# Kernel optimization log

Hardware: AMD Instinct MI355X
Metric: run time of the kernel (lower is better)

The kernel has to match this reference:

```python
import jax, jax.numpy as jnp
import numpy as np

EPS = jnp.float16(1e-8)

def setup_inputs() -> dict:
    key = jax.random.key(0)
    k1, k2, k3, k4 = jax.random.split(key, 4)
    B, S, D_IN, D_OUT = 4, 2048, 4096, 4096
    x = jax.random.normal(k1, (B, S, D_IN), dtype=jnp.float16)
    weight = jax.random.randint(k2, (D_OUT, D_IN), -127, 127, dtype=jnp.int32).astype(jnp.int8)
    weight_scales = (jax.random.uniform(k3, (D_OUT,), dtype=jnp.float32) * 0.02 + 0.001).astype(jnp.float16)
    bias = (jax.random.normal(k4, (1, D_OUT), dtype=jnp.float32) * 0.01).astype(jnp.float16)
    return {"x": x, "weight": weight, "weight_scales": weight_scales, "bias": bias}

def fake_quant_per_token(x):
    # per-token absmax fake quant to int8 range, stays fp16
    scales = jnp.max(jnp.abs(x), axis=-1, keepdims=True) / jnp.float16(127.0)
    scales = jnp.maximum(scales, EPS)
    return jnp.round(x / scales) * scales

def reference(x, weight, weight_scales, bias):
    # dequantize int8 weight with per-output-channel scales -> fp16 [out, in]
    w_fp16 = weight.astype(jnp.float16) * weight_scales[:, None]
    xq = fake_quant_per_token(x)
    # y = xq @ w^T + bias  : [B, S, out]
    y = jnp.einsum('bsi,oi->bso', xq, w_fp16) + bias
    return y
```

## Files before the change

kernel.cpp:

```cpp
#include <hip/hip_runtime.h>
#include <hip/hip_fp16.h>
#include <stdint.h>

#define M_TOK 8192
#define KD 4096
#define ND 4096

using i32x4 = __attribute__((ext_vector_type(4))) int;

typedef const __attribute__((address_space(1))) void* gp_t;
typedef __attribute__((address_space(3))) void* lp_t;

__global__ __launch_bounds__(256) void prep_kernel(
    const float* __restrict__ x,
    int8_t* __restrict__ q,
    float* __restrict__ scales,
    const int* __restrict__ w32,
    int8_t* __restrict__ w8)
{
    const int t = threadIdx.x;
    if (blockIdx.x >= 8192) {
        const int b = blockIdx.x - 8192;
        const int4* w4 = (const int4*)w32;
        int* q32 = (int*)w8;
        #pragma unroll
        for (int u = 0; u < 4; ++u) {
            int g = b * 1024 + u * 256 + t;
            int4 a = w4[g];
            q32[g] = (a.x & 255) | ((a.y & 255) << 8) | ((a.z & 255) << 16) | (a.w << 24);
        }
        return;
    }

    const int row  = blockIdx.x;
    const int lane = t & 63;
    const int wave = t >> 6;

    const float4* xr = (const float4*)(x + (size_t)row * KD);
    float4 p[4];
    #pragma unroll
    for (int i = 0; i < 4; ++i) p[i] = xr[i * 256 + t];

    float am = 0.0f;
    #pragma unroll
    for (int i = 0; i < 4; ++i) {
        am = fmaxf(am, fmaxf(fmaxf(fabsf(p[i].x), fabsf(p[i].y)),
                             fmaxf(fabsf(p[i].z), fabsf(p[i].w))));
    }
    #pragma unroll
    for (int off = 32; off >= 1; off >>= 1)
        am = fmaxf(am, __shfl_xor(am, off));

    __shared__ float smax[4];
    if (lane == 0) smax[wave] = am;
    __syncthreads();
    am = fmaxf(fmaxf(smax[0], smax[1]), fmaxf(smax[2], smax[3]));

    float s = __half2float(__float2half(am * (1.0f / 127.0f)));
    s = fmaxf(s, 1e-30f);
    const float inv = 1.0f / s;

    int* qr = (int*)(q + (size_t)row * KD);
    #pragma unroll
    for (int i = 0; i < 4; ++i) {
        float vv[4] = {p[i].x, p[i].y, p[i].z, p[i].w};
        int w32v = 0;
        #pragma unroll
        for (int e = 0; e < 4; ++e) {
            float tq = __half2float(__float2half(vv[e] * inv));
            int qi = (int)rintf(tq);
            qi = max(-127, min(127, qi));
            w32v |= (qi & 255) << (8 * e);
        }
        qr[i * 256 + t] = w32v;
    }
    if (t == 0) scales[row] = s;
}


template<int MH>
__device__ __forceinline__ void read_A(const char* lA, int wr, int lane, i32x4 (&a)[4][2]) {
    const int l15 = lane & 15;
    const int cg  = (lane >> 4) << 4;
    #pragma unroll
    for (int mf = 0; mf < 4; ++mf) {
        const int row = MH * 128 + wr * 64 + mf * 16 + l15;
        const int sw  = (row & 7) << 4;
        #pragma unroll
        for (int ks = 0; ks < 2; ++ks)
            a[mf][ks] = *(const i32x4*)(lA + row * 128 + ((ks * 64 + cg) ^ sw));
    }
}

template<int NH>
__device__ __forceinline__ void read_B(const char* lB, int wc, int lane, i32x4 (&b)[2][2]) {
    const int l15 = lane & 15;
    const int cg  = (lane >> 4) << 4;
    #pragma unroll
    for (int nf = 0; nf < 2; ++nf) {
        const int row = NH * 128 + wc * 32 + nf * 16 + l15;
        const int sw  = (row & 7) << 4;
        #pragma unroll
        for (int ks = 0; ks < 2; ++ks)
            b[nf][ks] = *(const i32x4*)(lB + row * 128 + ((ks * 64 + cg) ^ sw));
    }
}

template<int MH>
__device__ __forceinline__ void mfma_half(i32x4 (&acc)[2][4][2][2],
                                          const i32x4 (&a)[4][2],
                                          const i32x4 (&b0)[2][2],
                                          const i32x4 (&b1)[2][2]) {
    __builtin_amdgcn_s_setprio(1);
    #pragma unroll
    for (int ks = 0; ks < 2; ++ks)
        #pragma unroll
        for (int mf = 0; mf < 4; ++mf) {
            #pragma unroll
            for (int nf = 0; nf < 2; ++nf)
                acc[MH][mf][0][nf] =
                    __builtin_amdgcn_mfma_i32_16x16x64_i8(a[mf][ks], b0[nf][ks],
                                                          acc[MH][mf][0][nf], 0, 0, 0);
            #pragma unroll
            for (int nf = 0; nf < 2; ++nf)
                acc[MH][mf][1][nf] =
                    __builtin_amdgcn_mfma_i32_16x16x64_i8(a[mf][ks], b1[nf][ks],
                                                          acc[MH][mf][1][nf], 0, 0, 0);
        }
    __builtin_amdgcn_s_setprio(0);
}

#define BAR() do { __builtin_amdgcn_s_barrier(); __builtin_amdgcn_sched_barrier(0); } while (0)

__global__ __launch_bounds__(512, 2) void gemm_q8_4ph_kernel(
    const int8_t* __restrict__ q,
    const int8_t* __restrict__ w8,
    const float* __restrict__ qs,
    const float* __restrict__ wscale,
    const float* __restrict__ bias,
    float* __restrict__ y)
{
    __shared__ char lds[2][2][32768];

    const int tid  = threadIdx.x;
    const int lane = tid & 63;
    const int wave = tid >> 6;
    const int wr   = wave >> 2;
    const int wc   = wave & 3;
    const int tn   = blockIdx.x;
    const int tm   = blockIdx.y;

    const int8_t* gA = q  + (size_t)(tm * 256) * KD;
    const int8_t* gB = w8 + (size_t)(tn * 256) * KD;

    char* lA0 = &lds[0][0][0]; char* lB0 = &lds[0][1][0];
    char* lA1 = &lds[1][0][0]; char* lB1 = &lds[1][1][0];

    int goff[2];
    #pragma unroll
    for (int qq = 0; qq < 2; ++qq) {
        const int d = qq * 8192 + wave * 1024 + lane * 16;
        const int r = d >> 7;
        const int cs = (d & 127) ^ ((r & 7) << 4);
        goff[qq] = r * KD + cs;
    }
    const int ldso = wave * 1024;

    #define STAGE(gbase, half, kbyte, ldst)                                              \
        do {                                                                             \
            const int8_t* _s = (gbase) + (size_t)(half) * 128 * KD + (kbyte);            \
            __builtin_amdgcn_global_load_lds((gp_t)(_s + goff[0]),                       \
                (lp_t)((ldst) + (half) * 16384 + ldso), 16, 0, 0);                       \
            __builtin_amdgcn_global_load_lds((gp_t)(_s + goff[1]),                       \
                (lp_t)((ldst) + (half) * 16384 + 8192 + ldso), 16, 0, 0);                \
        } while (0)

    i32x4 acc[2][4][2][2] = {};
    i32x4 a[4][2], b0[2][2], b1[2][2];

    STAGE(gA, 0, 0,   lA0);
    STAGE(gB, 0, 0,   lB0);
    STAGE(gA, 1, 0,   lA0);
    STAGE(gB, 1, 0,   lB0);
    STAGE(gA, 0, 128, lA1);
    STAGE(gB, 0, 128, lB1);
    asm volatile("s_waitcnt vmcnt(4)");
    BAR();

    for (int it = 0; it < 16; ++it) {
        const int kt  = 2 * it;
        const int kb1 = ((kt + 1) & 31) * 128;
        const int kb2 = ((kt + 2) & 31) * 128;
        const int kb3 = ((kt + 3) & 31) * 128;

        read_A<0>(lA0, wr, lane, a);
        read_B<0>(lB0, wc, lane, b0);
        read_B<1>(lB0, wc, lane, b1);
        STAGE(gA, 1, kb1, lA1);
        STAGE(gB, 1, kb1, lB1);
        BAR();
        mfma_half<0>(acc, a, b0, b1);
        BAR();

        read_A<1>(lA0, wr, lane, a);
        STAGE(gA, 0, kb2, lA0);
        STAGE(gB, 0, kb2, lB0);
        BAR();
        mfma_half<1>(acc, a, b0, b1);
        asm volatile("s_waitcnt vmcnt(4)");
        BAR();

        read_A<0>(lA1, wr, lane, a);
        read_B<0>(lB1, wc, lane, b0);
        read_B<1>(lB1, wc, lane, b1);
        STAGE(gA, 1, kb2, lA0);
        STAGE(gB, 1, kb2, lB0);
        BAR();
        mfma_half<0>(acc, a, b0, b1);
        BAR();

        read_A<1>(lA1, wr, lane, a);
        STAGE(gA, 0, kb3, lA1);
        STAGE(gB, 0, kb3, lB1);
        BAR();
        mfma_half<1>(acc, a, b0, b1);
        asm volatile("s_waitcnt vmcnt(4)");
        BAR();
    }
    asm volatile("s_waitcnt vmcnt(0)");

    #pragma unroll
    for (int mh = 0; mh < 2; ++mh)
        #pragma unroll
        for (int mf = 0; mf < 4; ++mf) {
            const int rm = tm * 256 + mh * 128 + wr * 64 + mf * 16 + ((lane >> 4) << 2);
            float qsv[4];
            #pragma unroll
            for (int r = 0; r < 4; ++r) qsv[r] = qs[rm + r];
            #pragma unroll
            for (int nh = 0; nh < 2; ++nh)
                #pragma unroll
                for (int nf = 0; nf < 2; ++nf) {
                    const int n = tn * 256 + nh * 128 + wc * 32 + nf * 16 + (lane & 15);
                    const float wn = wscale[n];
                    const float bn = bias[n];
                    #pragma unroll
                    for (int r = 0; r < 4; ++r)
                        y[(size_t)(rm + r) * ND + n] =
                            (float)acc[mh][mf][nh][nf][r] * (qsv[r] * wn) + bn;
                }
        }
    #undef STAGE
}

__global__ __launch_bounds__(256, 2) void gemm_q8_fallback(
    const int8_t* __restrict__ q,
    const int* __restrict__ w32,
    const float* __restrict__ qs,
    const float* __restrict__ wscale,
    const float* __restrict__ bias,
    float* __restrict__ y)
{
    __shared__ int8_t lA[128 * 64];
    __shared__ int8_t lB[128 * 64];

    const int tid  = threadIdx.x;
    const int lane = tid & 63;
    const int wave = tid >> 6;
    const int wr   = wave >> 1;
    const int wc   = wave & 1;
    const int tn   = blockIdx.x;
    const int tm   = blockIdx.y;

    const int ci0  = wave * 2;
    const int off0 = ci0 * 1024 + lane * 16;
    const int r0   = off0 >> 6;
    const int c0   = off0 & 63;
    const int off1 = off0 + 1024;
    const int r1   = off1 >> 6;
    const int c1   = off1 & 63;

    const int8_t* gA0 = q + (size_t)(tm * 128 + r0) * KD + c0;
    const int8_t* gA1 = q + (size_t)(tm * 128 + r1) * KD + c1;

    const int brow  = tid >> 1;
    const int bhalf = tid & 1;
    const int* gW = w32 + (size_t)(tn * 128 + brow) * KD + bhalf * 32;

    i32x4 acc[4][4] = {};
    const int kc = (lane >> 4) * 16;
    const int rA = wr * 64 + (lane & 15);
    const int rB = wc * 64 + (lane & 15);

    for (int k0 = 0; k0 < KD; k0 += 64) {
        __builtin_amdgcn_global_load_lds((gp_t)(gA0 + k0), (lp_t)(lA + ci0 * 1024),        16, 0, 0);
        __builtin_amdgcn_global_load_lds((gp_t)(gA1 + k0), (lp_t)(lA + ci0 * 1024 + 1024), 16, 0, 0);
        int bw[8];
        #pragma unroll
        for (int u = 0; u < 8; ++u) {
            i32x4 a4 = *(const i32x4*)(gW + k0 + u * 4);
            bw[u] = (a4[0] & 255) | ((a4[1] & 255) << 8) | ((a4[2] & 255) << 16) | (a4[3] << 24);
        }
        *(i32x4*)(lB + brow * 64 + bhalf * 32)      = i32x4{bw[0], bw[1], bw[2], bw[3]};
        *(i32x4*)(lB + brow * 64 + bhalf * 32 + 16) = i32x4{bw[4], bw[5], bw[6], bw[7]};
        __syncthreads();

        i32x4 a[4], b[4];
        #pragma unroll
        for (int i = 0; i < 4; ++i) a[i] = *(const i32x4*)(lA + (rA + i * 16) * 64 + kc);
        #pragma unroll
        for (int j = 0; j < 4; ++j) b[j] = *(const i32x4*)(lB + (rB + j * 16) * 64 + kc);
        #pragma unroll
        for (int i = 0; i < 4; ++i)
            #pragma unroll
            for (int j = 0; j < 4; ++j)
                acc[i][j] = __builtin_amdgcn_mfma_i32_16x16x64_i8(a[i], b[j], acc[i][j], 0, 0, 0);
        __syncthreads();
    }

    const int cbase = tn * 128 + wc * 64 + (lane & 15);
    const int rbase = tm * 128 + wr * 64 + ((lane >> 4) << 2);
    #pragma unroll
    for (int j = 0; j < 4; ++j) {
        const int n  = cbase + j * 16;
        const float wn = wscale[n];
        const float bn = bias[n];
        #pragma unroll
        for (int i = 0; i < 4; ++i)
            #pragma unroll
            for (int r = 0; r < 4; ++r) {
                const int m = rbase + i * 16 + r;
                y[(size_t)m * ND + n] = (float)acc[i][j][r] * (qs[m] * wn) + bn;
            }
    }
}

extern "C" void kernel_launch(void* const* d_in, const int* in_sizes, int n_in,
                              void* d_out, int out_size, void* d_ws, size_t ws_size,
                              hipStream_t stream) {
    const float* x      = (const float*)d_in[0];
    const int*   w32    = (const int*)d_in[1];
    const float* wscale = (const float*)d_in[2];
    const float* bias   = (const float*)d_in[3];
    float*       y      = (float*)d_out;

    const size_t q_bytes  = (size_t)M_TOK * KD;
    const size_t s_bytes  = (size_t)M_TOK * sizeof(float);
    const size_t w8_bytes = (size_t)ND * KD;

    int8_t* qbuf   = (int8_t*)d_ws;
    float*  scales = (float*)((char*)d_ws + q_bytes);
    int8_t* w8     = (int8_t*)((char*)d_ws + q_bytes + s_bytes);

    if (ws_size >= q_bytes + s_bytes + w8_bytes) {
        prep_kernel<<<8192 + 4096, 256, 0, stream>>>(x, qbuf, scales, w32, w8);
        dim3 grid(ND / 256, M_TOK / 256);
        gemm_q8_4ph_kernel<<<grid, 512, 0, stream>>>(qbuf, w8, scales, wscale, bias, y);
    } else {
        prep_kernel<<<8192, 256, 0, stream>>>(x, qbuf, scales, w32, w8);
        dim3 grid(ND / 128, M_TOK / 128);
        gemm_q8_fallback<<<grid, 256, 0, stream>>>(qbuf, w32, scales, wscale, bias, y);
    }
}
```

Before: 181.9 us.

## Switch int8 GEMM from 16x16x64 to 32x32x32 MFMA tiles

Replaces the 16x16x64 int8 MFMA instructions with 32x32x32 int8 MFMA. Each wave now covers a 64x64 N-slice per M-half instead of two 32-wide N-halves. The LDS read patterns, the per-wave tile mapping and the epilogue indexing are rewritten to match the 32x32 accumulator layout. The aim is to cut LDS operand reads per MAC and reuse B fragments across both M-halves. The risk is that the larger accumulator vectors raise register pressure and change LDS bank access.

```diff
diff --git a/kernel.cpp b/kernel.cpp
--- a/kernel.cpp
+++ b/kernel.cpp
@@ -6,7 +6,8 @@
 #define KD 4096
 #define ND 4096
 
-using i32x4 = __attribute__((ext_vector_type(4))) int;
+using i32x4  = __attribute__((ext_vector_type(4))) int;
+using i32x16 = __attribute__((ext_vector_type(16))) int;
 
 typedef const __attribute__((address_space(1))) void* gp_t;
 typedef __attribute__((address_space(3))) void* lp_t;
@@ -79,60 +80,52 @@
 
 
 template<int MH>
-__device__ __forceinline__ void read_A(const char* lA, int wr, int lane, i32x4 (&a)[4][2]) {
-    const int l15 = lane & 15;
-    const int cg  = (lane >> 4) << 4;
-    #pragma unroll
-    for (int mf = 0; mf < 4; ++mf) {
-        const int row = MH * 128 + wr * 64 + mf * 16 + l15;
+__device__ __forceinline__ void read_A32(const char* lA, int wr, int lane, i32x4 (&a)[2][4]) {
+    const int l31 = lane & 31;
+    const int kc  = (lane >> 5) << 4;
+    #pragma unroll
+    for (int mf = 0; mf < 2; ++mf) {
+        const int row = MH * 128 + wr * 64 + mf * 32 + l31;
         const int sw  = (row & 7) << 4;
         #pragma unroll
-        for (int ks = 0; ks < 2; ++ks)
-            a[mf][ks] = *(const i32x4*)(lA + row * 128 + ((ks * 64 + cg) ^ sw));
-    }
-}
-
-template<int NH>
-__device__ __forceinline__ void read_B(const char* lB, int wc, int lane, i32x4 (&b)[2][2]) {
-    const int l15 = lane & 15;
-    const int cg  = (lane >> 4) << 4;
+        for (int ks = 0; ks < 4; ++ks)
+            a[mf][ks] = *(const i32x4*)(lA + row * 128 + ((ks * 32 + kc) ^ sw));
+    }
+}
+
+__device__ __forceinline__ void read_B32(const char* lB, int wc, int lane, i32x4 (&b)[2][4]) {
+    const int l31 = lane & 31;
+    const int kc  = (lane >> 5) << 4;
     #pragma unroll
     for (int nf = 0; nf < 2; ++nf) {
-        const int row = NH * 128 + wc * 32 + nf * 16 + l15;
+        const int row = wc * 64 + nf * 32 + l31;
         const int sw  = (row & 7) << 4;
         #pragma unroll
-        for (int ks = 0; ks < 2; ++ks)
-            b[nf][ks] = *(const i32x4*)(lB + row * 128 + ((ks * 64 + cg) ^ sw));
+        for (int ks = 0; ks < 4; ++ks)
+            b[nf][ks] = *(const i32x4*)(lB + row * 128 + ((ks * 32 + kc) ^ sw));
     }
 }
 
 template<int MH>
-__device__ __forceinline__ void mfma_half(i32x4 (&acc)[2][4][2][2],
-                                          const i32x4 (&a)[4][2],
-                                          const i32x4 (&b0)[2][2],
-                                          const i32x4 (&b1)[2][2]) {
+__device__ __forceinline__ void mfma_half32(i32x16 (&acc)[2][2][2],
+                                            const i32x4 (&a)[2][4],
+                                            const i32x4 (&b)[2][4]) {
     __builtin_amdgcn_s_setprio(1);
     #pragma unroll
-    for (int ks = 0; ks < 2; ++ks)
-        #pragma unroll
-        for (int mf = 0; mf < 4; ++mf) {
+    for (int ks = 0; ks < 4; ++ks)
+        #pragma unroll
+        for (int mf = 0; mf < 2; ++mf)
             #pragma unroll
             for (int nf = 0; nf < 2; ++nf)
-                acc[MH][mf][0][nf] =
-                    __builtin_amdgcn_mfma_i32_16x16x64_i8(a[mf][ks], b0[nf][ks],
-                                                          acc[MH][mf][0][nf], 0, 0, 0);
-            #pragma unroll
-            for (int nf = 0; nf < 2; ++nf)
-                acc[MH][mf][1][nf] =
-                    __builtin_amdgcn_mfma_i32_16x16x64_i8(a[mf][ks], b1[nf][ks],
-                                                          acc[MH][mf][1][nf], 0, 0, 0);
-        }
+                acc[MH][mf][nf] =
+                    __builtin_amdgcn_mfma_i32_32x32x32_i8(a[mf][ks], b[nf][ks],
+                                                          acc[MH][mf][nf], 0, 0, 0);
     __builtin_amdgcn_s_setprio(0);
 }
 
 #define BAR() do { __builtin_amdgcn_s_barrier(); __builtin_amdgcn_sched_barrier(0); } while (0)
 
-__global__ __launch_bounds__(512, 2) void gemm_q8_4ph_kernel(
+__global__ __launch_bounds__(512, 2) void gemm_q8_32x32_kernel(
     const int8_t* __restrict__ q,
     const int8_t* __restrict__ w8,
     const float* __restrict__ qs,
@@ -175,8 +168,8 @@
                 (lp_t)((ldst) + (half) * 16384 + 8192 + ldso), 16, 0, 0);                \
         } while (0)
 
-    i32x4 acc[2][4][2][2] = {};
-    i32x4 a[4][2], b0[2][2], b1[2][2];
+    i32x16 acc[2][2][2] = {};
+    i32x4 a[2][4], b[2][4];
 
     STAGE(gA, 0, 0,   lA0);
     STAGE(gB, 0, 0,   lB0);
@@ -193,37 +186,35 @@
         const int kb2 = ((kt + 2) & 31) * 128;
         const int kb3 = ((kt + 3) & 31) * 128;
 
-        read_A<0>(lA0, wr, lane, a);
-        read_B<0>(lB0, wc, lane, b0);
-        read_B<1>(lB0, wc, lane, b1);
+        read_A32<0>(lA0, wr, lane, a);
+        read_B32(lB0, wc, lane, b);
         STAGE(gA, 1, kb1, lA1);
         STAGE(gB, 1, kb1, lB1);
         BAR();
-        mfma_half<0>(acc, a, b0, b1);
-        BAR();
-
-        read_A<1>(lA0, wr, lane, a);
+        mfma_half32<0>(acc, a, b);
+        BAR();
+
+        read_A32<1>(lA0, wr, lane, a);
         STAGE(gA, 0, kb2, lA0);
         STAGE(gB, 0, kb2, lB0);
         BAR();
-        mfma_half<1>(acc, a, b0, b1);
+        mfma_half32<1>(acc, a, b);
         asm volatile("s_waitcnt vmcnt(4)");
         BAR();
 
-        read_A<0>(lA1, wr, lane, a);
-        read_B<0>(lB1, wc, lane, b0);
-        read_B<1>(lB1, wc, lane, b1);
+        read_A32<0>(lA1, wr, lane, a);
+        read_B32(lB1, wc, lane, b);
         STAGE(gA, 1, kb2, lA0);
         STAGE(gB, 1, kb2, lB0);
         BAR();
-        mfma_half<0>(acc, a, b0, b1);
-        BAR();
-
-        read_A<1>(lA1, wr, lane, a);
+        mfma_half32<0>(acc, a, b);
+        BAR();
+
+        read_A32<1>(lA1, wr, lane, a);
         STAGE(gA, 0, kb3, lA1);
         STAGE(gB, 0, kb3, lB1);
         BAR();
-        mfma_half<1>(acc, a, b0, b1);
+        mfma_half32<1>(acc, a, b);
         asm volatile("s_waitcnt vmcnt(4)");
         BAR();
     }
@@ -232,23 +223,24 @@
     #pragma unroll
     for (int mh = 0; mh < 2; ++mh)
         #pragma unroll
-        for (int mf = 0; mf < 4; ++mf) {
-            const int rm = tm * 256 + mh * 128 + wr * 64 + mf * 16 + ((lane >> 4) << 2);
-            float qsv[4];
-            #pragma unroll
-            for (int r = 0; r < 4; ++r) qsv[r] = qs[rm + r];
-            #pragma unroll
-            for (int nh = 0; nh < 2; ++nh)
+        for (int mf = 0; mf < 2; ++mf) {
+            const int rbase = tm * 256 + mh * 128 + wr * 64 + mf * 32 + ((lane >> 5) << 2);
+            float qsv[16];
+            #pragma unroll
+            for (int reg = 0; reg < 16; ++reg)
+                qsv[reg] = qs[rbase + (reg & 3) + 8 * (reg >> 2)];
+            #pragma unroll
+            for (int nf = 0; nf < 2; ++nf) {
+                const int n = tn * 256 + wc * 64 + nf * 32 + (lane & 31);
+                const float wn = wscale[n];
+                const float bn = bias[n];
                 #pragma unroll
-                for (int nf = 0; nf < 2; ++nf) {
-                    const int n = tn * 256 + nh * 128 + wc * 32 + nf * 16 + (lane & 15);
-                    const float wn = wscale[n];
-                    const float bn = bias[n];
-                    #pragma unroll
-                    for (int r = 0; r < 4; ++r)
-                        y[(size_t)(rm + r) * ND + n] =
-                            (float)acc[mh][mf][nh][nf][r] * (qsv[r] * wn) + bn;
+                for (int reg = 0; reg < 16; ++reg) {
+                    const int m = rbase + (reg & 3) + 8 * (reg >> 2);
+                    y[(size_t)m * ND + n] =
+                        (float)acc[mh][mf][nf][reg] * (qsv[reg] * wn) + bn;
                 }
+            }
         }
     #undef STAGE
 }
@@ -355,7 +347,7 @@
     if (ws_size >= q_bytes + s_bytes + w8_bytes) {
         prep_kernel<<<8192 + 4096, 256, 0, stream>>>(x, qbuf, scales, w32, w8);
         dim3 grid(ND / 256, M_TOK / 256);
-        gemm_q8_4ph_kernel<<<grid, 512, 0, stream>>>(qbuf, w8, scales, wscale, bias, y);
+        gemm_q8_32x32_kernel<<<grid, 512, 0, stream>>>(qbuf, w8, scales, wscale, bias, y);
     } else {
         prep_kernel<<<8192, 256, 0, stream>>>(x, qbuf, scales, w32, w8);
         dim3 grid(ND / 128, M_TOK / 128);
```

New measurement: 196.9 us. 8.2% more time.

## Peel final K iteration and stage epilogue through swizzled LDS for vector stores

Applied to the files above, without the earlier changes.

The last main-loop iteration is peeled so it no longer issues wrap-around prefetches of K tiles that are never used. The epilogue writes scaled accumulators into a per-wave XOR-swizzled LDS region. It then reads them back as 16-byte rows and writes coalesced float4 nontemporal stores to the output, instead of scattered 4-byte stores. This cuts wasted global loads and improves write coalescing, at the cost of extra LDS traffic and barriers in the epilogue.

```diff
diff --git a/kernel.cpp b/kernel.cpp
--- a/kernel.cpp
+++ b/kernel.cpp
@@ -7,6 +7,7 @@
 #define ND 4096
 
 using i32x4 = __attribute__((ext_vector_type(4))) int;
+using f32x4 = __attribute__((ext_vector_type(4))) float;
 
 typedef const __attribute__((address_space(1))) void* gp_t;
 typedef __attribute__((address_space(3))) void* lp_t;
@@ -187,11 +188,11 @@
     asm volatile("s_waitcnt vmcnt(4)");
     BAR();
 
-    for (int it = 0; it < 16; ++it) {
+    for (int it = 0; it < 15; ++it) {
         const int kt  = 2 * it;
-        const int kb1 = ((kt + 1) & 31) * 128;
-        const int kb2 = ((kt + 2) & 31) * 128;
-        const int kb3 = ((kt + 3) & 31) * 128;
+        const int kb1 = (kt + 1) * 128;
+        const int kb2 = (kt + 2) * 128;
+        const int kb3 = (kt + 3) * 128;
 
         read_A<0>(lA0, wr, lane, a);
         read_B<0>(lB0, wc, lane, b0);
@@ -227,29 +228,77 @@
         asm volatile("s_waitcnt vmcnt(4)");
         BAR();
     }
-    asm volatile("s_waitcnt vmcnt(0)");
-
-    #pragma unroll
-    for (int mh = 0; mh < 2; ++mh)
-        #pragma unroll
-        for (int mf = 0; mf < 4; ++mf) {
-            const int rm = tm * 256 + mh * 128 + wr * 64 + mf * 16 + ((lane >> 4) << 2);
-            float qsv[4];
-            #pragma unroll
-            for (int r = 0; r < 4; ++r) qsv[r] = qs[rm + r];
-            #pragma unroll
-            for (int nh = 0; nh < 2; ++nh)
+
+    {
+        const int kb1 = 31 * 128;
+        read_A<0>(lA0, wr, lane, a);
+        read_B<0>(lB0, wc, lane, b0);
+        read_B<1>(lB0, wc, lane, b1);
+        STAGE(gA, 1, kb1, lA1);
+        STAGE(gB, 1, kb1, lB1);
+        BAR();
+        mfma_half<0>(acc, a, b0, b1);
+        BAR();
+
+        read_A<1>(lA0, wr, lane, a);
+        BAR();
+        mfma_half<1>(acc, a, b0, b1);
+        asm volatile("s_waitcnt vmcnt(0)");
+        BAR();
+
+        read_A<0>(lA1, wr, lane, a);
+        read_B<0>(lB1, wc, lane, b0);
+        read_B<1>(lB1, wc, lane, b1);
+        BAR();
+        mfma_half<0>(acc, a, b0, b1);
+        BAR();
+
+        read_A<1>(lA1, wr, lane, a);
+        BAR();
+        mfma_half<1>(acc, a, b0, b1);
+        BAR();
+    }
+
+    {
+        char* myl = &lds[0][0][0] + wave * 16384;
+        const int g   = lane >> 4;
+        const int l15 = lane & 15;
+        #pragma unroll
+        for (int nh = 0; nh < 2; ++nh) {
+            #pragma unroll
+            for (int mh = 0; mh < 2; ++mh)
                 #pragma unroll
-                for (int nf = 0; nf < 2; ++nf) {
-                    const int n = tn * 256 + nh * 128 + wc * 32 + nf * 16 + (lane & 15);
-                    const float wn = wscale[n];
-                    const float bn = bias[n];
+                for (int mf = 0; mf < 4; ++mf) {
+                    const int rmb = tm * 256 + mh * 128 + wr * 64 + mf * 16 + g * 4;
+                    float qsv[4];
                     #pragma unroll
-                    for (int r = 0; r < 4; ++r)
-                        y[(size_t)(rm + r) * ND + n] =
-                            (float)acc[mh][mf][nh][nf][r] * (qsv[r] * wn) + bn;
+                    for (int r = 0; r < 4; ++r) qsv[r] = qs[rmb + r];
+                    #pragma unroll
+                    for (int nf = 0; nf < 2; ++nf) {
+                        const int n  = tn * 256 + nh * 128 + wc * 32 + nf * 16 + l15;
+                        const float wn = wscale[n];
+                        const float bn = bias[n];
+                        const int cl = nf * 16 + l15;
+                        #pragma unroll
+                        for (int r = 0; r < 4; ++r) {
+                            const int rl = mh * 64 + mf * 16 + g * 4 + r;
+                            const float val = (float)acc[mh][mf][nh][nf][r] * (qsv[r] * wn) + bn;
+                            *(float*)(myl + rl * 128 + ((cl * 4) ^ ((rl & 7) << 4))) = val;
+                        }
+                    }
                 }
+            __builtin_amdgcn_s_barrier();
+            const int gcol = tn * 256 + nh * 128 + wc * 32 + (lane & 7) * 4;
+            #pragma unroll
+            for (int k = 0; k < 16; ++k) {
+                const int rl = (lane >> 3) + k * 8;
+                const f32x4 v = *(const f32x4*)(myl + rl * 128 + (((lane & 7) * 16) ^ ((rl & 7) << 4)));
+                const int grow = tm * 256 + (rl >> 6) * 128 + wr * 64 + (rl & 63);
+                __builtin_nontemporal_store(v, (f32x4*)(y + (size_t)grow * ND + gcol));
+            }
+            __builtin_amdgcn_s_barrier();
         }
+    }
     #undef STAGE
 }
 
```

Result: faster. 167.8 us (-7.8%).

## Replace 256x256 8-wave GEMM with 128x128 4-wave tile and LDS-staged epilogue

Applied to the files above, without the earlier changes.

Swaps the 256x256-tile, 512-thread int8 GEMM for a 128x128-tile, 256-thread kernel. Each wave now computes a 64x64 sub-tile over a simpler two-phase double-buffered loop with explicit lgkm/vm waits. The epilogue is rewritten to stage the scaled outputs through swizzled LDS and write them with coalesced 16-byte nontemporal stores. The smaller tile roughly doubles global operand traffic per FLOP and reduces reuse, in exchange for more blocks, smaller LDS use and better store coalescing.

```diff
diff --git a/kernel.cpp b/kernel.cpp
--- a/kernel.cpp
+++ b/kernel.cpp
@@ -7,6 +7,7 @@
 #define ND 4096
 
 using i32x4 = __attribute__((ext_vector_type(4))) int;
+using f32x4 = __attribute__((ext_vector_type(4))) float;
 
 typedef const __attribute__((address_space(1))) void* gp_t;
 typedef __attribute__((address_space(3))) void* lp_t;
@@ -78,13 +79,12 @@
 }
 
 
-template<int MH>
-__device__ __forceinline__ void read_A(const char* lA, int wr, int lane, i32x4 (&a)[4][2]) {
+__device__ __forceinline__ void read_Af(const char* lA, int wr, int lane, i32x4 (&a)[4][2]) {
     const int l15 = lane & 15;
     const int cg  = (lane >> 4) << 4;
     #pragma unroll
     for (int mf = 0; mf < 4; ++mf) {
-        const int row = MH * 128 + wr * 64 + mf * 16 + l15;
+        const int row = wr * 64 + mf * 16 + l15;
         const int sw  = (row & 7) << 4;
         #pragma unroll
         for (int ks = 0; ks < 2; ++ks)
@@ -92,13 +92,12 @@
     }
 }
 
-template<int NH>
-__device__ __forceinline__ void read_B(const char* lB, int wc, int lane, i32x4 (&b)[2][2]) {
+__device__ __forceinline__ void read_Bf(const char* lB, int wc, int lane, i32x4 (&b)[4][2]) {
     const int l15 = lane & 15;
     const int cg  = (lane >> 4) << 4;
     #pragma unroll
-    for (int nf = 0; nf < 2; ++nf) {
-        const int row = NH * 128 + wc * 32 + nf * 16 + l15;
+    for (int nf = 0; nf < 4; ++nf) {
+        const int row = wc * 64 + nf * 16 + l15;
         const int sw  = (row & 7) << 4;
         #pragma unroll
         for (int ks = 0; ks < 2; ++ks)
@@ -106,33 +105,26 @@
     }
 }
 
-template<int MH>
-__device__ __forceinline__ void mfma_half(i32x4 (&acc)[2][4][2][2],
-                                          const i32x4 (&a)[4][2],
-                                          const i32x4 (&b0)[2][2],
-                                          const i32x4 (&b1)[2][2]) {
+__device__ __forceinline__ void mfma_32(i32x4 (&acc)[4][4],
+                                        const i32x4 (&a)[4][2],
+                                        const i32x4 (&b)[4][2]) {
     __builtin_amdgcn_s_setprio(1);
     #pragma unroll
     for (int ks = 0; ks < 2; ++ks)
         #pragma unroll
-        for (int mf = 0; mf < 4; ++mf) {
-            #pragma unroll
-            for (int nf = 0; nf < 2; ++nf)
-                acc[MH][mf][0][nf] =
-                    __builtin_amdgcn_mfma_i32_16x16x64_i8(a[mf][ks], b0[nf][ks],
-                                                          acc[MH][mf][0][nf], 0, 0, 0);
-            #pragma unroll
-            for (int nf = 0; nf < 2; ++nf)
-                acc[MH][mf][1][nf] =
-                    __builtin_amdgcn_mfma_i32_16x16x64_i8(a[mf][ks], b1[nf][ks],
-                                                          acc[MH][mf][1][nf], 0, 0, 0);
-        }
+        for (int mf = 0; mf < 4; ++mf)
+            #pragma unroll
+            for (int nf = 0; nf < 4; ++nf)
+                acc[mf][nf] = __builtin_amdgcn_mfma_i32_16x16x64_i8(a[mf][ks], b[nf][ks],
+                                                                    acc[mf][nf], 0, 0, 0);
     __builtin_amdgcn_s_setprio(0);
 }
 
-#define BAR() do { __builtin_amdgcn_s_barrier(); __builtin_amdgcn_sched_barrier(0); } while (0)
-
-__global__ __launch_bounds__(512, 2) void gemm_q8_4ph_kernel(
+#define BAR()   __builtin_amdgcn_s_barrier()
+#define LGKM0() asm volatile("s_waitcnt lgkmcnt(0)" ::: "memory")
+#define VM8()   asm volatile("s_waitcnt vmcnt(8)")
+
+__global__ __launch_bounds__(256, 2) void gemm_q8_128_kernel(
     const int8_t* __restrict__ q,
     const int8_t* __restrict__ w8,
     const float* __restrict__ qs,
@@ -140,116 +132,113 @@
     const float* __restrict__ bias,
     float* __restrict__ y)
 {
-    __shared__ char lds[2][2][32768];
+    __shared__ char lds[2][2][16384];
 
     const int tid  = threadIdx.x;
     const int lane = tid & 63;
     const int wave = tid >> 6;
-    const int wr   = wave >> 2;
-    const int wc   = wave & 3;
+    const int wr   = wave >> 1;
+    const int wc   = wave & 1;
     const int tn   = blockIdx.x;
     const int tm   = blockIdx.y;
 
-    const int8_t* gA = q  + (size_t)(tm * 256) * KD;
-    const int8_t* gB = w8 + (size_t)(tn * 256) * KD;
+    const int8_t* gA = q  + (size_t)(tm * 128) * KD;
+    const int8_t* gB = w8 + (size_t)(tn * 128) * KD;
 
     char* lA0 = &lds[0][0][0]; char* lB0 = &lds[0][1][0];
     char* lA1 = &lds[1][0][0]; char* lB1 = &lds[1][1][0];
 
-    int goff[2];
-    #pragma unroll
-    for (int qq = 0; qq < 2; ++qq) {
-        const int d = qq * 8192 + wave * 1024 + lane * 16;
+    int goff[4];
+    #pragma unroll
+    for (int ch = 0; ch < 4; ++ch) {
+        const int d = ch * 4096 + tid * 16;
         const int r = d >> 7;
         const int cs = (d & 127) ^ ((r & 7) << 4);
-        goff[qq] = r * KD + cs;
-    }
-    const int ldso = wave * 1024;
-
-    #define STAGE(gbase, half, kbyte, ldst)                                              \
+        goff[ch] = r * KD + cs;
+    }
+    const int ldso = tid * 16;
+
+    #define STAGE(gbase, kbyte, ldst)                                                    \
         do {                                                                             \
-            const int8_t* _s = (gbase) + (size_t)(half) * 128 * KD + (kbyte);            \
-            __builtin_amdgcn_global_load_lds((gp_t)(_s + goff[0]),                       \
-                (lp_t)((ldst) + (half) * 16384 + ldso), 16, 0, 0);                       \
-            __builtin_amdgcn_global_load_lds((gp_t)(_s + goff[1]),                       \
-                (lp_t)((ldst) + (half) * 16384 + 8192 + ldso), 16, 0, 0);                \
+            const int8_t* _s = (gbase) + (kbyte);                                        \
+            __builtin_amdgcn_global_load_lds((gp_t)(_s + goff[0]), (lp_t)((ldst) + ldso),            16, 0, 0); \
+            __builtin_amdgcn_global_load_lds((gp_t)(_s + goff[1]), (lp_t)((ldst) + 4096 + ldso),     16, 0, 0); \
+            __builtin_amdgcn_global_load_lds((gp_t)(_s + goff[2]), (lp_t)((ldst) + 8192 + ldso),     16, 0, 0); \
+            __builtin_amdgcn_global_load_lds((gp_t)(_s + goff[3]), (lp_t)((ldst) + 12288 + ldso),    16, 0, 0); \
         } while (0)
 
-    i32x4 acc[2][4][2][2] = {};
-    i32x4 a[4][2], b0[2][2], b1[2][2];
-
-    STAGE(gA, 0, 0,   lA0);
-    STAGE(gB, 0, 0,   lB0);
-    STAGE(gA, 1, 0,   lA0);
-    STAGE(gB, 1, 0,   lB0);
-    STAGE(gA, 0, 128, lA1);
-    STAGE(gB, 0, 128, lB1);
-    asm volatile("s_waitcnt vmcnt(4)");
+    i32x4 acc[4][4] = {};
+    i32x4 a[4][2], b[4][2];
+
+    STAGE(gA, 0,   lA0);
+    STAGE(gB, 0,   lB0);
+    STAGE(gA, 128, lA1);
+    STAGE(gB, 128, lB1);
+    VM8();
     BAR();
 
     for (int it = 0; it < 16; ++it) {
         const int kt  = 2 * it;
-        const int kb1 = ((kt + 1) & 31) * 128;
         const int kb2 = ((kt + 2) & 31) * 128;
         const int kb3 = ((kt + 3) & 31) * 128;
 
-        read_A<0>(lA0, wr, lane, a);
-        read_B<0>(lB0, wc, lane, b0);
-        read_B<1>(lB0, wc, lane, b1);
-        STAGE(gA, 1, kb1, lA1);
-        STAGE(gB, 1, kb1, lB1);
+        read_Af(lA0, wr, lane, a);
+        read_Bf(lB0, wc, lane, b);
+        LGKM0();
         BAR();
-        mfma_half<0>(acc, a, b0, b1);
+        STAGE(gA, kb2, lA0);
+        STAGE(gB, kb2, lB0);
+        mfma_32(acc, a, b);
+        VM8();
         BAR();
 
-        read_A<1>(lA0, wr, lane, a);
-        STAGE(gA, 0, kb2, lA0);
-        STAGE(gB, 0, kb2, lB0);
+        read_Af(lA1, wr, lane, a);
+        read_Bf(lB1, wc, lane, b);
+        LGKM0();
         BAR();
-        mfma_half<1>(acc, a, b0, b1);
-        asm volatile("s_waitcnt vmcnt(4)");
+        STAGE(gA, kb3, lA1);
+        STAGE(gB, kb3, lB1);
+        mfma_32(acc, a, b);
+        VM8();
         BAR();
-
-        read_A<0>(lA1, wr, lane, a);
-        read_B<0>(lB1, wc, lane, b0);
-        read_B<1>(lB1, wc, lane, b1);
-        STAGE(gA, 1, kb2, lA0);
-        STAGE(gB, 1, kb2, lB0);
-        BAR();
-        mfma_half<0>(acc, a, b0, b1);
-        BAR();
-
-        read_A<1>(lA1, wr, lane, a);
-        STAGE(gA, 0, kb3, lA1);
-        STAGE(gB, 0, kb3, lB1);
-        BAR();
-        mfma_half<1>(acc, a, b0, b1);
-        asm volatile("s_waitcnt vmcnt(4)");
-        BAR();
     }
     asm volatile("s_waitcnt vmcnt(0)");
-
-    #pragma unroll
-    for (int mh = 0; mh < 2; ++mh)
+    BAR();
+
+    {
+        char* myl = &lds[0][0][0] + wave * 16384;
+        const int g   = lane >> 4;
+        const int l15 = lane & 15;
         #pragma unroll
         for (int mf = 0; mf < 4; ++mf) {
-            const int rm = tm * 256 + mh * 128 + wr * 64 + mf * 16 + ((lane >> 4) << 2);
+            const int rmb = tm * 128 + wr * 64 + mf * 16 + g * 4;
             float qsv[4];
             #pragma unroll
-            for (int r = 0; r < 4; ++r) qsv[r] = qs[rm + r];
-            #pragma unroll
-            for (int nh = 0; nh < 2; ++nh)
+            for (int r = 0; r < 4; ++r) qsv[r] = qs[rmb + r];
+            #pragma unroll
+            for (int nf = 0; nf < 4; ++nf) {
+                const int n  = tn * 128 + wc * 64 + nf * 16 + l15;
+                const float wn = wscale[n];
+                const float bn = bias[n];
+                const int cl = nf * 16 + l15;
                 #pragma unroll
-                for (int nf = 0; nf < 2; ++nf) {
-                    const int n = tn * 256 + nh * 128 + wc * 32 + nf * 16 + (lane & 15);
-                    const float wn = wscale[n];
-                    const float bn = bias[n];
-                    #pragma unroll
-                    for (int r = 0; r < 4; ++r)
-                        y[(size_t)(rm + r) * ND + n] =
-                            (float)acc[mh][mf][nh][nf][r] * (qsv[r] * wn) + bn;
+                for (int r = 0; r < 4; ++r) {
+                    const int rl = mf * 16 + g * 4 + r;
+                    const float val = (float)acc[mf][nf][r] * (qsv[r] * wn) + bn;
+                    *(float*)(myl + rl * 256 + ((cl * 4) ^ ((rl & 7) << 4))) = val;
                 }
-        }
+            }
+        }
+        __builtin_amdgcn_s_barrier();
+        const int gcol = tn * 128 + wc * 64 + l15 * 4;
+        #pragma unroll
+        for (int k = 0; k < 16; ++k) {
+            const int rl = g + k * 4;
+            const f32x4 v = *(const f32x4*)(myl + rl * 256 + ((l15 * 16) ^ ((rl & 7) << 4)));
+            const int grow = tm * 128 + wr * 64 + rl;
+            __builtin_nontemporal_store(v, (f32x4*)(y + (size_t)grow * ND + gcol));
+        }
+    }
     #undef STAGE
 }
 
@@ -354,8 +343,8 @@
 
     if (ws_size >= q_bytes + s_bytes + w8_bytes) {
         prep_kernel<<<8192 + 4096, 256, 0, stream>>>(x, qbuf, scales, w32, w8);
-        dim3 grid(ND / 256, M_TOK / 256);
-        gemm_q8_4ph_kernel<<<grid, 512, 0, stream>>>(qbuf, w8, scales, wscale, bias, y);
+        dim3 grid(ND / 128, M_TOK / 128);
+        gemm_q8_128_kernel<<<grid, 256, 0, stream>>>(qbuf, w8, scales, wscale, bias, y);
     } else {
         prep_kernel<<<8192, 256, 0, stream>>>(x, qbuf, scales, w32, w8);
         dim3 grid(ND / 128, M_TOK / 128);
```

Result: faster. 174.0 us (-4.4%).
